# Optimization experiments

Measured on AMD Instinct MI355X. Metric: run time of the kernel, lower is better.

## Reference

```python
import jax, jax.numpy as jnp
import numpy as np

# RBF_Conv2d config (matches init_kwargs)
KH = KW = 3
STRIDE = 1
OUT_CH = 256
IN_CH = 64
STD = 2.0  # gauss RBF std (activate_param[0])


def setup_inputs() -> dict:
    key = jax.random.key(0)
    k1, k2 = jax.random.split(key)
    x = jax.random.normal(k1, (16, IN_CH, 56, 56), dtype=jnp.float32)
    # kaiming_uniform_ on fan_in = IN_CH*KH*KW = 576 -> bound = sqrt(6/576)
    bound = float(np.sqrt(6.0 / (IN_CH * KH * KW)))
    weight = jax.random.uniform(k2, (OUT_CH, IN_CH * KH * KW), dtype=jnp.float32,
                                minval=-bound, maxval=bound)
    return {"x": x, "weight": weight}


def _cdist_conv(x, weight):
    # im2col: [B, C*KH*KW, Ho, Wo]; channel ordering (c, kh, kw) matches F.unfold
    patches = jax.lax.conv_general_dilated_patches(
        x, (KH, KW), (STRIDE, STRIDE), 'VALID')
    B, Kdim, Ho, Wo = patches.shape
    win = patches.reshape(B, Kdim, Ho * Wo).transpose(0, 2, 1)  # [B, P, K]
    # Euclidean distance via the expansion ||w||^2 + ||c||^2 - 2 w.c (no [B,P,K,O] tensor)
    w2 = jnp.sum(win * win, axis=-1, keepdims=True)            # [B, P, 1]
    c2 = jnp.sum(weight * weight, axis=-1)[None, None, :]      # [1, 1, O]
    d2 = w2 + c2 - 2.0 * jnp.einsum('bpk,ok->bpo', win, weight)
    dist = jnp.sqrt(jnp.maximum(d2, 1e-12))                    # [B, P, O]
    return dist, (B, Ho, Wo)


def reference(x, weight):
    dist, (B, Ho, Wo) = _cdist_conv(x, weight)
    # gauss RBF: exp(-d^2 / (2*std^2))
    act = jnp.exp(-(dist * dist) / (2.0 * STD * STD))
    # permute back to [B, O, Ho, Wo] like the torch code
    return act.transpose(0, 2, 1).reshape(B, OUT_CH, Ho, Wo)
```

## Files before the change

### kernel.cpp

```cpp
#include <hip/hip_runtime.h>
#include <hip/hip_bf16.h>
#include <stdint.h>

#define BATCH 16
#define IN_CH 64
#define HIN 56
#define WIN_ 56
#define HO 54
#define WO 54
#define P_PER_B (HO*WO)
#define P_PAD 2944
#define OUT_CH 256
#define KDIM 576
#define NPIX (HIN*WIN_)

typedef __attribute__((ext_vector_type(8))) short short8;
typedef __attribute__((ext_vector_type(4))) float f32x4;

__device__ __forceinline__ unsigned short f2bf(float f) {
    unsigned int u = __float_as_uint(f);
    unsigned int r = (u + 0x7fffu + ((u >> 16) & 1u)) >> 16;
    return (unsigned short)r;
}


__global__ void prep_weight(const float* __restrict__ w, short* __restrict__ wbf,
                            float* __restrict__ c2) {
    int o = blockIdx.x;
    int lane = threadIdx.x;
    float s = 0.f;
    #pragma unroll
    for (int j = 0; j < 9; ++j) {
        int k = j * 64 + lane;
        int c = k / 9, tap = k % 9;
        float v = w[o * KDIM + k];
        s += v * v;
        ((unsigned short*)wbf)[o * KDIM + tap * 64 + c] = f2bf(v);
    }
    #pragma unroll
    for (int off = 32; off > 0; off >>= 1) s += __shfl_down(s, off);
    if (lane == 0) c2[o] = s;
}

__global__ __launch_bounds__(256) void transpose_kernel(
    const float* __restrict__ x, short* __restrict__ xT, float* __restrict__ s) {
    __shared__ short lds[64 * 65];
    __shared__ float red[256];
    const int b    = blockIdx.x / 49;
    const int pix0 = (blockIdx.x % 49) * 64;
    const int tid  = threadIdx.x;
    const int quarter = tid >> 6;
    const int pix  = tid & 63;
    const float* xb = x + (size_t)b * IN_CH * NPIX + pix0 + pix;
    float acc = 0.f;
    #pragma unroll
    for (int it = 0; it < 16; ++it) {
        int c = quarter * 16 + it;
        float v = xb[c * NPIX];
        acc += v * v;
        lds[pix * 65 + c] = (short)f2bf(v);
    }
    red[tid] = acc;
    __syncthreads();
    const int cs = tid & 63;
    short* xTb = xT + ((size_t)b * NPIX + pix0) * 64;
    #pragma unroll
    for (int it = 0; it < 16; ++it) {
        int pixs = quarter * 16 + it;
        xTb[(size_t)pixs * 64 + cs] = lds[pixs * 65 + cs];
    }
    if (tid < 64)
        s[b * NPIX + pix0 + tid] = red[tid] + red[64 + tid] + red[128 + tid] + red[192 + tid];
}

__global__ void w2_kernel(const float* __restrict__ s, float* __restrict__ w2) {
    int t = blockIdx.x * 256 + threadIdx.x;
    if (t >= BATCH * P_PER_B) return;
    int b = t / P_PER_B, p = t % P_PER_B;
    int oh = p / WO, ow = p % WO;
    const float* sp = s + b * NPIX + oh * WIN_ + ow;
    float acc = 0.f;
    #pragma unroll
    for (int kh = 0; kh < 3; ++kh)
        #pragma unroll
        for (int kw = 0; kw < 3; ++kw)
            acc += sp[kh * WIN_ + kw];
    w2[b * P_PAD + p] = acc;
}


#define AS1(p) ((const __attribute__((address_space(1))) void*)(p))
#define AS3(p) ((__attribute__((address_space(3))) void*)(p))

__constant__ int dtab[9] = {0, 1, 2, 56, 57, 58, 112, 113, 114};

__global__ __launch_bounds__(256) void gemm_rbf(
    const short* __restrict__ xT, const short* __restrict__ wbf,
    const float* __restrict__ w2, const float* __restrict__ c2,
    float* __restrict__ out) {
    __shared__ __align__(16) short lds_a[128 * 64];
    __shared__ __align__(16) short lds_b[128 * 64];

    const int mt = blockIdx.x;
    const int b  = mt / 23;
    const int p0 = (mt % 23) * 128;
    const int n0 = blockIdx.y * 128;

    const int tid  = threadIdx.x;
    const int wave = tid >> 6;
    const int lane = tid & 63;
    const int r16  = lane & 15;
    const int quad = lane >> 4;
    const int wm = (wave >> 1) * 64;
    const int wn = (wave & 1) * 64;

    const int srow = lane >> 3;
    const int scx  = (lane & 7) ^ srow;

    const short* xTb = xT + (size_t)b * NPIX * 64;

    const short* gaB[4];
    const short* gbB[4];
    #pragma unroll
    for (int i = 0; i < 4; ++i) {
        int row = (wave * 4 + i) * 8 + srow;
        int p = p0 + row;
        if (p > P_PER_B - 1) p = P_PER_B - 1;
        int oh = p / WO, ow = p - oh * WO;
        gaB[i] = xTb + (size_t)(oh * WIN_ + ow) * 64 + scx * 8;
        gbB[i] = wbf + (size_t)(n0 + row) * KDIM + scx * 8;
    }
    const int xq = r16 & 7;

    f32x4 acc[4][4];
    #pragma unroll
    for (int i = 0; i < 4; ++i)
        #pragma unroll
        for (int j = 0; j < 4; ++j)
            acc[i][j] = (f32x4){0.f, 0.f, 0.f, 0.f};

    #pragma unroll
    for (int kt = 0; kt < 9; ++kt) {
        const int doff = dtab[kt];
        #pragma unroll
        for (int i = 0; i < 4; ++i) {
            int rb = wave * 4 + i;
            __builtin_amdgcn_global_load_lds(AS1(gaB[i] + doff * 64),
                                             AS3(lds_a + rb * 512), 16, 0, 0);
            __builtin_amdgcn_global_load_lds(AS1(gbB[i] + kt * 64),
                                             AS3(lds_b + rb * 512), 16, 0, 0);
        }
        __syncthreads();
        #pragma unroll
        for (int ks = 0; ks < 2; ++ks) {
            short8 af[4], bfr[4];
            #pragma unroll
            for (int ms = 0; ms < 4; ++ms)
                af[ms] = *(const short8*)(lds_a + (wm + ms * 16 + r16) * 64
                                                + (((ks * 4 + quad) ^ xq) * 8));
            #pragma unroll
            for (int ns = 0; ns < 4; ++ns)
                bfr[ns] = *(const short8*)(lds_b + (wn + ns * 16 + r16) * 64
                                                 + (((ks * 4 + quad) ^ xq) * 8));
            #pragma unroll
            for (int ms = 0; ms < 4; ++ms)
                #pragma unroll
                for (int ns = 0; ns < 4; ++ns)
                    acc[ms][ns] = __builtin_amdgcn_mfma_f32_16x16x32_bf16(
                        af[ms], bfr[ns], acc[ms][ns], 0, 0, 0);
        }
        __syncthreads();
    }

    #pragma unroll
    for (int ms = 0; ms < 4; ++ms) {
        int pl = wm + ms * 16 + quad * 4;
        int p  = p0 + pl;
        if (p >= P_PER_B) continue;
        f32x4 w2v = *(const f32x4*)(w2 + b * P_PAD + p);
        bool full = (p + 3 < P_PER_B);
        #pragma unroll
        for (int ns = 0; ns < 4; ++ns) {
            int o = n0 + wn + ns * 16 + r16;
            float c2o = c2[o];
            f32x4 v;
            #pragma unroll
            for (int r = 0; r < 4; ++r) {
                float d2 = w2v[r] + c2o - 2.0f * acc[ms][ns][r];
                d2 = fmaxf(d2, 1e-12f);
                v[r] = __expf(-0.125f * d2);
            }
            float* outp = out + ((size_t)(b * OUT_CH + o)) * P_PER_B + p;
            if (full) {
                *(f32x4*)outp = v;
            } else {
                #pragma unroll
                for (int r = 0; r < 4; ++r)
                    if (p + r < P_PER_B) outp[r] = v[r];
            }
        }
    }
}


extern "C" void kernel_launch(void* const* d_in, const int* in_sizes, int n_in,
                              void* d_out, int out_size, void* d_ws, size_t ws_size,
                              hipStream_t stream) {
    const float* x = (const float*)d_in[0];
    const float* w = (const float*)d_in[1];
    float* out = (float*)d_out;

    char* ws = (char*)d_ws;
    const size_t wbf_bytes = (size_t)OUT_CH * KDIM * 2;
    const size_t c2_bytes  = 1024;
    const size_t w2_bytes  = (size_t)BATCH * P_PAD * 4;
    const size_t s_bytes   = (size_t)BATCH * NPIX * 4;
    short* wbf = (short*)ws;
    float* c2  = (float*)(ws + wbf_bytes);
    float* w2  = (float*)(ws + wbf_bytes + c2_bytes);
    float* s   = (float*)(ws + wbf_bytes + c2_bytes + w2_bytes);
    short* xT  = (short*)(ws + wbf_bytes + c2_bytes + w2_bytes + s_bytes);

    hipLaunchKernelGGL(prep_weight, dim3(OUT_CH), dim3(64), 0, stream, w, wbf, c2);
    hipLaunchKernelGGL(transpose_kernel, dim3(16 * 49), dim3(256), 0, stream, x, xT, s);
    hipLaunchKernelGGL(w2_kernel, dim3((BATCH * P_PER_B + 255) / 256), dim3(256), 0, stream, s, w2);
    hipLaunchKernelGGL(gemm_rbf, dim3(23 * BATCH, OUT_CH / 128), dim3(256), 0, stream,
                       xT, wbf, w2, c2, out);
}
```

Measured before the change: 105.1 us.

## Double-buffer LDS tiles in RBF GEMM to overlap loads with MFMA

Splits the A and B shared-memory tiles into two buffers. The next K-slice's global-to-LDS DMA loads are issued before the MFMAs on the current slice run, and the trailing barrier is dropped so there is one sync per iteration. The aim is to hide global load latency behind compute. In exchange, LDS per block doubles to 64KB, which can lower how many blocks fit on a CU, and the compiler may still insert conservative waits on the async LDS loads that cut into the overlap.

```diff
diff --git a/kernel.cpp b/kernel.cpp
--- a/kernel.cpp
+++ b/kernel.cpp
@@ -98,8 +98,8 @@
     const short* __restrict__ xT, const short* __restrict__ wbf,
     const float* __restrict__ w2, const float* __restrict__ c2,
     float* __restrict__ out) {
-    __shared__ __align__(16) short lds_a[128 * 64];
-    __shared__ __align__(16) short lds_b[128 * 64];
+    __shared__ __align__(16) short lds_a[2][128 * 64];
+    __shared__ __align__(16) short lds_b[2][128 * 64];
 
     const int mt = blockIdx.x;
     const int b  = mt / 23;
@@ -116,6 +116,7 @@
 
     const int srow = lane >> 3;
     const int scx  = (lane & 7) ^ srow;
+    const int rb   = wave * 4;
 
     const short* xTb = xT + (size_t)b * NPIX * 64;
 
@@ -123,7 +124,7 @@
     const short* gbB[4];
     #pragma unroll
     for (int i = 0; i < 4; ++i) {
-        int row = (wave * 4 + i) * 8 + srow;
+        int row = (rb + i) * 8 + srow;
         int p = p0 + row;
         if (p > P_PER_B - 1) p = P_PER_B - 1;
         int oh = p / WO, ow = p - oh * WO;
@@ -140,28 +141,38 @@
             acc[i][j] = (f32x4){0.f, 0.f, 0.f, 0.f};
 
     #pragma unroll
+    for (int i = 0; i < 4; ++i) {
+        __builtin_amdgcn_global_load_lds(AS1(gaB[i] + dtab[0] * 64),
+                                         AS3(&lds_a[0][(rb + i) * 512]), 16, 0, 0);
+        __builtin_amdgcn_global_load_lds(AS1(gbB[i] + 0 * 64),
+                                         AS3(&lds_b[0][(rb + i) * 512]), 16, 0, 0);
+    }
+
+    #pragma unroll
     for (int kt = 0; kt < 9; ++kt) {
-        const int doff = dtab[kt];
-        #pragma unroll
-        for (int i = 0; i < 4; ++i) {
-            int rb = wave * 4 + i;
-            __builtin_amdgcn_global_load_lds(AS1(gaB[i] + doff * 64),
-                                             AS3(lds_a + rb * 512), 16, 0, 0);
-            __builtin_amdgcn_global_load_lds(AS1(gbB[i] + kt * 64),
-                                             AS3(lds_b + rb * 512), 16, 0, 0);
+        const int cur = kt & 1, nxt = cur ^ 1;
+        __syncthreads();
+        if (kt < 8) {
+            const int doff = dtab[kt + 1];
+            #pragma unroll
+            for (int i = 0; i < 4; ++i) {
+                __builtin_amdgcn_global_load_lds(AS1(gaB[i] + doff * 64),
+                                                 AS3(&lds_a[nxt][(rb + i) * 512]), 16, 0, 0);
+                __builtin_amdgcn_global_load_lds(AS1(gbB[i] + (kt + 1) * 64),
+                                                 AS3(&lds_b[nxt][(rb + i) * 512]), 16, 0, 0);
+            }
         }
-        __syncthreads();
         #pragma unroll
         for (int ks = 0; ks < 2; ++ks) {
             short8 af[4], bfr[4];
             #pragma unroll
             for (int ms = 0; ms < 4; ++ms)
-                af[ms] = *(const short8*)(lds_a + (wm + ms * 16 + r16) * 64
-                                                + (((ks * 4 + quad) ^ xq) * 8));
+                af[ms] = *(const short8*)(&lds_a[cur][(wm + ms * 16 + r16) * 64
+                                                + (((ks * 4 + quad) ^ xq) * 8)]);
             #pragma unroll
             for (int ns = 0; ns < 4; ++ns)
-                bfr[ns] = *(const short8*)(lds_b + (wn + ns * 16 + r16) * 64
-                                                 + (((ks * 4 + quad) ^ xq) * 8));
+                bfr[ns] = *(const short8*)(&lds_b[cur][(wn + ns * 16 + r16) * 64
+                                                 + (((ks * 4 + quad) ^ xq) * 8)]);
             #pragma unroll
             for (int ms = 0; ms < 4; ++ms)
                 #pragma unroll
@@ -169,7 +180,6 @@
                     acc[ms][ns] = __builtin_amdgcn_mfma_f32_16x16x32_bf16(
                         af[ms], bfr[ns], acc[ms][ns], 0, 0, 0);
         }
-        __syncthreads();
     }
 
     #pragma unroll
```

Result: slower. 114.9 us (+9.3%).

## Load GEMM fragments directly from global into registers with double buffering

Applied to the files above, without the earlier changes.

Drops the LDS staging in gemm_rbf. Each wave now loads its A and B MFMA fragments straight from global memory into registers, with a two-stage register double buffer across the 9 kernel taps, and the block barriers are gone. Block indexing is remapped so consecutive blocks cover different batches, and launch bounds ask for 2 blocks per CU. Sharing operands within a block now happens only through L1/L2 rather than LDS, which raises global traffic and register pressure.

```diff
diff --git a/kernel.cpp b/kernel.cpp
--- a/kernel.cpp
+++ b/kernel.cpp
@@ -89,21 +89,15 @@
 }
 
 
-#define AS1(p) ((const __attribute__((address_space(1))) void*)(p))
-#define AS3(p) ((__attribute__((address_space(3))) void*)(p))
-
-__constant__ int dtab[9] = {0, 1, 2, 56, 57, 58, 112, 113, 114};
-
-__global__ __launch_bounds__(256) void gemm_rbf(
+__global__ __launch_bounds__(256, 2) void gemm_rbf(
     const short* __restrict__ xT, const short* __restrict__ wbf,
     const float* __restrict__ w2, const float* __restrict__ c2,
     float* __restrict__ out) {
-    __shared__ __align__(16) short lds_a[128 * 64];
-    __shared__ __align__(16) short lds_b[128 * 64];
-
-    const int mt = blockIdx.x;
-    const int b  = mt / 23;
-    const int p0 = (mt % 23) * 128;
+    constexpr int dtab[9] = {0, 1, 2, 56, 57, 58, 112, 113, 114};
+
+    const int bx = blockIdx.x;
+    const int b  = bx & 15;
+    const int p0 = (bx >> 4) * 128;
     const int n0 = blockIdx.y * 128;
 
     const int tid  = threadIdx.x;
@@ -114,23 +108,20 @@
     const int wm = (wave >> 1) * 64;
     const int wn = (wave & 1) * 64;
 
-    const int srow = lane >> 3;
-    const int scx  = (lane & 7) ^ srow;
-
     const short* xTb = xT + (size_t)b * NPIX * 64;
 
-    const short* gaB[4];
-    const short* gbB[4];
-    #pragma unroll
-    for (int i = 0; i < 4; ++i) {
-        int row = (wave * 4 + i) * 8 + srow;
-        int p = p0 + row;
+    const short* aB[4];
+    const short* bB[4];
+    #pragma unroll
+    for (int ms = 0; ms < 4; ++ms) {
+        int p = p0 + wm + ms * 16 + r16;
         if (p > P_PER_B - 1) p = P_PER_B - 1;
         int oh = p / WO, ow = p - oh * WO;
-        gaB[i] = xTb + (size_t)(oh * WIN_ + ow) * 64 + scx * 8;
-        gbB[i] = wbf + (size_t)(n0 + row) * KDIM + scx * 8;
-    }
-    const int xq = r16 & 7;
+        aB[ms] = xTb + (size_t)(oh * WIN_ + ow) * 64 + quad * 8;
+    }
+    #pragma unroll
+    for (int ns = 0; ns < 4; ++ns)
+        bB[ns] = wbf + (size_t)(n0 + wn + ns * 16 + r16) * KDIM + quad * 8;
 
     f32x4 acc[4][4];
     #pragma unroll
@@ -139,37 +130,41 @@
         for (int j = 0; j < 4; ++j)
             acc[i][j] = (f32x4){0.f, 0.f, 0.f, 0.f};
 
-    #pragma unroll
-    for (int kt = 0; kt < 9; ++kt) {
-        const int doff = dtab[kt];
-        #pragma unroll
-        for (int i = 0; i < 4; ++i) {
-            int rb = wave * 4 + i;
-            __builtin_amdgcn_global_load_lds(AS1(gaB[i] + doff * 64),
-                                             AS3(lds_a + rb * 512), 16, 0, 0);
-            __builtin_amdgcn_global_load_lds(AS1(gbB[i] + kt * 64),
-                                             AS3(lds_b + rb * 512), 16, 0, 0);
+    short8 Af[2][4][2], Bf[2][4][2];
+    #pragma unroll
+    for (int ms = 0; ms < 4; ++ms)
+        #pragma unroll
+        for (int ks = 0; ks < 2; ++ks)
+            Af[0][ms][ks] = *(const short8*)(aB[ms] + dtab[0] * 64 + ks * 32);
+    #pragma unroll
+    for (int ns = 0; ns < 4; ++ns)
+        #pragma unroll
+        for (int ks = 0; ks < 2; ++ks)
+            Bf[0][ns][ks] = *(const short8*)(bB[ns] + ks * 32);
+
+    #pragma unroll
+    for (int t = 0; t < 9; ++t) {
+        const int cur = t & 1, nxt = cur ^ 1;
+        if (t < 8) {
+            #pragma unroll
+            for (int ms = 0; ms < 4; ++ms)
+                #pragma unroll
+                for (int ks = 0; ks < 2; ++ks)
+                    Af[nxt][ms][ks] = *(const short8*)(aB[ms] + dtab[t + 1] * 64 + ks * 32);
+            #pragma unroll
+            for (int ns = 0; ns < 4; ++ns)
+                #pragma unroll
+                for (int ks = 0; ks < 2; ++ks)
+                    Bf[nxt][ns][ks] = *(const short8*)(bB[ns] + (t + 1) * 64 + ks * 32);
         }
-        __syncthreads();
-        #pragma unroll
-        for (int ks = 0; ks < 2; ++ks) {
-            short8 af[4], bfr[4];
-            #pragma unroll
-            for (int ms = 0; ms < 4; ++ms)
-                af[ms] = *(const short8*)(lds_a + (wm + ms * 16 + r16) * 64
-                                                + (((ks * 4 + quad) ^ xq) * 8));
-            #pragma unroll
-            for (int ns = 0; ns < 4; ++ns)
-                bfr[ns] = *(const short8*)(lds_b + (wn + ns * 16 + r16) * 64
-                                                 + (((ks * 4 + quad) ^ xq) * 8));
+        #pragma unroll
+        for (int ks = 0; ks < 2; ++ks)
             #pragma unroll
             for (int ms = 0; ms < 4; ++ms)
                 #pragma unroll
                 for (int ns = 0; ns < 4; ++ns)
                     acc[ms][ns] = __builtin_amdgcn_mfma_f32_16x16x32_bf16(
-                        af[ms], bfr[ns], acc[ms][ns], 0, 0, 0);
-        }
-        __syncthreads();
+                        Af[cur][ms][ks], Bf[cur][ns][ks], acc[ms][ns], 0, 0, 0);
     }
 
     #pragma unroll
```

Result: slower. 138.4 us (+31.6%).
